# Performance work log

Measured on AMD Instinct MI355X. Metric: run time of the kernel, lower is better.

## Reference

```python
import jax, jax.numpy as jnp
import numpy as np

HIDDEN_DIM = 4096
NUM_SHARDS = 64
TOP_K = 2
B = 16384


def setup_inputs() -> dict:
    key = jax.random.key(0)
    k_h, k_w = jax.random.split(key)
    h = jax.random.normal(k_h, (B, HIDDEN_DIM), dtype=jnp.float32)
    # nn.init.normal_(weight, std=0.02); bias zeros
    weight = jax.random.normal(k_w, (NUM_SHARDS, HIDDEN_DIM), dtype=jnp.float32) * 0.02
    bias = jnp.zeros((NUM_SHARDS,), dtype=jnp.float32)
    return {"h": h, "weight": weight, "bias": bias}


def reference(h, weight, bias):
    # logits: (B, num_shards)
    logits = jnp.einsum("bd,ed->be", h, weight) + bias
    probs = jax.nn.softmax(logits, axis=-1)
    k = min(TOP_K, weight.shape[0])
    topk_vals, topk_idx = jax.lax.top_k(probs, k)
    denom = jnp.maximum(jnp.sum(topk_vals, axis=-1, keepdims=True), 1e-12)
    topk_w = topk_vals / denom
    return topk_w, topk_idx
```

## Files before the change

kernel.cpp:

```cpp
#include <hip/hip_runtime.h>
#include <hip/hip_bf16.h>
#include <math.h>


#define HIDDEN 4096
#define NSHARD 64
#define B_ROWS 16384

typedef short bf16x8 __attribute__((ext_vector_type(8)));
typedef float f32x4  __attribute__((ext_vector_type(4)));

__device__ __forceinline__ unsigned short f32_to_bf16_rn(float f) {
    __hip_bfloat16 h = __float2bfloat16(f);
    return *reinterpret_cast<unsigned short*>(&h);
}
__device__ __forceinline__ float bf16_bits_to_f32(unsigned short u) {
    union { unsigned int i; float f; } v; v.i = ((unsigned int)u) << 16;
    return v.f;
}

__global__ __launch_bounds__(256)
void wsplit_kernel(const float* __restrict__ w,
                   unsigned short* __restrict__ w_hi,
                   unsigned short* __restrict__ w_lo)
{
    const int idx = (blockIdx.x * 256 + threadIdx.x) * 4;
    const float4 v = *(const float4*)(w + idx);
    const float a[4] = {v.x, v.y, v.z, v.w};
    ushort4 hi, lo;
    unsigned short hb;
    hb = f32_to_bf16_rn(a[0]); hi.x = hb; lo.x = f32_to_bf16_rn(a[0] - bf16_bits_to_f32(hb));
    hb = f32_to_bf16_rn(a[1]); hi.y = hb; lo.y = f32_to_bf16_rn(a[1] - bf16_bits_to_f32(hb));
    hb = f32_to_bf16_rn(a[2]); hi.z = hb; lo.z = f32_to_bf16_rn(a[2] - bf16_bits_to_f32(hb));
    hb = f32_to_bf16_rn(a[3]); hi.w = hb; lo.w = f32_to_bf16_rn(a[3] - bf16_bits_to_f32(hb));
    *(ushort4*)(w_hi + idx) = hi;
    *(ushort4*)(w_lo + idx) = lo;
}

__global__ __launch_bounds__(256)
void gate_kernel(const float* __restrict__ h,
                 const unsigned short* __restrict__ w_hi,
                 const unsigned short* __restrict__ w_lo,
                 const float* __restrict__ bias,
                 float* __restrict__ out)
{
    __shared__ float lsum[4][16][68];

    const int tid  = threadIdx.x;
    const int lane = tid & 63;
    const int q    = tid >> 6;
    const int m    = lane & 15;
    const int quad = lane >> 4;
    const int row0 = blockIdx.x * 16;

    const float* __restrict__ aptr =
        h + (size_t)(row0 + m) * HIDDEN + q * 1024 + quad * 8;
    const size_t boff = (size_t)m * HIDDEN + q * 1024 + quad * 8;

    f32x4 acch[4], accx[4];
#pragma unroll
    for (int j = 0; j < 4; ++j) {
        acch[j] = (f32x4)0.0f;
        accx[j] = (f32x4)0.0f;
    }

    for (int step = 0; step < 32; ++step) {
        const float4 a0 = *(const float4*)(aptr + step * 32);
        const float4 a1 = *(const float4*)(aptr + step * 32 + 4);
        const float av[8] = {a0.x, a0.y, a0.z, a0.w, a1.x, a1.y, a1.z, a1.w};
        bf16x8 ahi, alo;
#pragma unroll
        for (int i = 0; i < 8; ++i) {
            const unsigned short hb = f32_to_bf16_rn(av[i]);
            ahi[i] = (short)hb;
            alo[i] = (short)f32_to_bf16_rn(av[i] - bf16_bits_to_f32(hb));
        }
#pragma unroll
        for (int j = 0; j < 4; ++j) {
            const bf16x8 bh = *(const bf16x8*)(w_hi + boff + (size_t)j * 16 * HIDDEN + step * 32);
            const bf16x8 bl = *(const bf16x8*)(w_lo + boff + (size_t)j * 16 * HIDDEN + step * 32);
            acch[j] = __builtin_amdgcn_mfma_f32_16x16x32_bf16(ahi, bh, acch[j], 0, 0, 0);
            accx[j] = __builtin_amdgcn_mfma_f32_16x16x32_bf16(alo, bh, accx[j], 0, 0, 0);
            accx[j] = __builtin_amdgcn_mfma_f32_16x16x32_bf16(ahi, bl, accx[j], 0, 0, 0);
            accx[j] = __builtin_amdgcn_mfma_f32_16x16x32_bf16(alo, bl, accx[j], 0, 0, 0);
        }
    }

#pragma unroll
    for (int j = 0; j < 4; ++j)
#pragma unroll
        for (int p = 0; p < 4; ++p)
            lsum[q][quad * 4 + p][j * 16 + m] = acch[j][p] + accx[j][p];

    __syncthreads();

    const int row = tid >> 4;
    const int s   = tid & 15;
    float4 vs = *(const float4*)&lsum[0][row][s * 4];
    {
        const float4 v1 = *(const float4*)&lsum[1][row][s * 4];
        const float4 v2 = *(const float4*)&lsum[2][row][s * 4];
        const float4 v3 = *(const float4*)&lsum[3][row][s * 4];
        vs.x += v1.x + v2.x + v3.x;
        vs.y += v1.y + v2.y + v3.y;
        vs.z += v1.z + v2.z + v3.z;
        vs.w += v1.w + v2.w + v3.w;
    }
    const float4 bv = *(const float4*)(bias + s * 4);
    const float v0 = vs.x + bv.x, v1 = vs.y + bv.y;
    const float v2 = vs.z + bv.z, v3 = vs.w + bv.w;

    float m1 = v0, m2 = -INFINITY;
    int   i1 = s * 4, i2 = 0;
    if (v1 > m1)      { m2 = m1; i2 = i1; m1 = v1; i1 = s * 4 + 1; }
    else              { m2 = v1; i2 = s * 4 + 1; }
    if (v2 > m1)      { m2 = m1; i2 = i1; m1 = v2; i1 = s * 4 + 2; }
    else if (v2 > m2) { m2 = v2; i2 = s * 4 + 2; }
    if (v3 > m1)      { m2 = m1; i2 = i1; m1 = v3; i1 = s * 4 + 3; }
    else if (v3 > m2) { m2 = v3; i2 = s * 4 + 3; }

#pragma unroll
    for (int msk = 1; msk <= 8; msk <<= 1) {
        const float o1 = __shfl_xor(m1, msk, 64);
        const int   q1 = __shfl_xor(i1, msk, 64);
        const float o2 = __shfl_xor(m2, msk, 64);
        const int   q2 = __shfl_xor(i2, msk, 64);
        const bool take = (o1 > m1) || (o1 == m1 && q1 < i1);
        const float w1 = take ? o1 : m1; const int w1i = take ? q1 : i1;
        const float l1 = take ? m1 : o1; const int l1i = take ? i1 : q1;
        const float s2 = take ? o2 : m2; const int s2i = take ? q2 : i2;
        const bool t2 = (l1 > s2) || (l1 == s2 && l1i < s2i);
        m1 = w1; i1 = w1i;
        m2 = t2 ? l1 : s2; i2 = t2 ? l1i : s2i;
    }

    if (s == 0) {
        const int orow = row0 + row;
        const float ed  = expf(m2 - m1);
        const float inv = 1.0f / (1.0f + ed);
        out[2 * orow + 0] = inv;
        out[2 * orow + 1] = ed * inv;
        float* __restrict__ oidx = out + 2 * B_ROWS;
        oidx[2 * orow + 0] = (float)i1;
        oidx[2 * orow + 1] = (float)i2;
    }
}

extern "C" void kernel_launch(void* const* d_in, const int* in_sizes, int n_in,
                              void* d_out, int out_size, void* d_ws, size_t ws_size,
                              hipStream_t stream)
{
    const float* h    = (const float*)d_in[0];
    const float* wt   = (const float*)d_in[1];
    const float* bias = (const float*)d_in[2];
    float* out = (float*)d_out;

    unsigned short* w_hi = (unsigned short*)d_ws;
    unsigned short* w_lo = w_hi + (size_t)NSHARD * HIDDEN;

    wsplit_kernel<<<dim3(NSHARD * HIDDEN / 1024), dim3(256), 0, stream>>>(wt, w_hi, w_lo);
    gate_kernel<<<dim3(B_ROWS / 16), dim3(256), 0, stream>>>(h, w_hi, w_lo, bias, out);
}
```

Before: 464.9 us.

## Split shard columns across twice the waves and fully unroll K loop

Doubles the block to 512 threads so each wave computes only two of the four 16-column shard tiles, halving the accumulators per wave and raising the number of waves per CU. The K loop is fully unrolled with all B-operand loads hoisted ahead of the split and MFMA work, and the bf16 hi/lo split is done with hand-written integer rounding. The cost is that each A tile is now loaded and split twice, once by each wave in a pair, which adds global traffic and VALU work.

```diff
diff --git a/kernel.cpp b/kernel.cpp
--- a/kernel.cpp
+++ b/kernel.cpp
@@ -19,6 +19,16 @@
     return v.f;
 }
 
+__device__ __forceinline__ void bf16_split(float f, short* hi, short* lo) {
+    const unsigned int u = __float_as_uint(f);
+    const unsigned int r = u + 0x7fffu + ((u >> 16) & 1u);
+    *hi = (short)(r >> 16);
+    union { unsigned int i; float f2; } hv; hv.i = r & 0xffff0000u;
+    const float res = f - hv.f2;
+    const unsigned int u2 = __float_as_uint(res);
+    *lo = (short)((u2 + 0x7fffu + ((u2 >> 16) & 1u)) >> 16);
+}
+
 __global__ __launch_bounds__(256)
 void wsplit_kernel(const float* __restrict__ w,
                    unsigned short* __restrict__ w_hi,
@@ -37,7 +47,7 @@
     *(ushort4*)(w_lo + idx) = lo;
 }
 
-__global__ __launch_bounds__(256)
+__global__ __launch_bounds__(512, 8)
 void gate_kernel(const float* __restrict__ h,
                  const unsigned short* __restrict__ w_hi,
                  const unsigned short* __restrict__ w_lo,
@@ -48,7 +58,9 @@
 
     const int tid  = threadIdx.x;
     const int lane = tid & 63;
-    const int q    = tid >> 6;
+    const int wv   = tid >> 6;
+    const int q    = wv >> 1;
+    const int jh   = wv & 1;
     const int m    = lane & 15;
     const int quad = lane >> 4;
     const int row0 = blockIdx.x * 16;
@@ -56,93 +68,106 @@
     const float* __restrict__ aptr =
         h + (size_t)(row0 + m) * HIDDEN + q * 1024 + quad * 8;
     const size_t boff = (size_t)m * HIDDEN + q * 1024 + quad * 8;
+    const unsigned short* __restrict__ bh0p = w_hi + boff + (size_t)(jh * 2 + 0) * 16 * HIDDEN;
+    const unsigned short* __restrict__ bh1p = w_hi + boff + (size_t)(jh * 2 + 1) * 16 * HIDDEN;
+    const unsigned short* __restrict__ bl0p = w_lo + boff + (size_t)(jh * 2 + 0) * 16 * HIDDEN;
+    const unsigned short* __restrict__ bl1p = w_lo + boff + (size_t)(jh * 2 + 1) * 16 * HIDDEN;
 
-    f32x4 acch[4], accx[4];
+    f32x4 acch[2], accx[2];
 #pragma unroll
-    for (int j = 0; j < 4; ++j) {
+    for (int j = 0; j < 2; ++j) {
         acch[j] = (f32x4)0.0f;
         accx[j] = (f32x4)0.0f;
     }
 
+#pragma unroll
     for (int step = 0; step < 32; ++step) {
         const float4 a0 = *(const float4*)(aptr + step * 32);
         const float4 a1 = *(const float4*)(aptr + step * 32 + 4);
+        const bf16x8 bh0 = *(const bf16x8*)(bh0p + step * 32);
+        const bf16x8 bh1 = *(const bf16x8*)(bh1p + step * 32);
+        const bf16x8 bl0 = *(const bf16x8*)(bl0p + step * 32);
+        const bf16x8 bl1 = *(const bf16x8*)(bl1p + step * 32);
+
         const float av[8] = {a0.x, a0.y, a0.z, a0.w, a1.x, a1.y, a1.z, a1.w};
         bf16x8 ahi, alo;
 #pragma unroll
         for (int i = 0; i < 8; ++i) {
-            const unsigned short hb = f32_to_bf16_rn(av[i]);
-            ahi[i] = (short)hb;
-            alo[i] = (short)f32_to_bf16_rn(av[i] - bf16_bits_to_f32(hb));
+            short hb, lb;
+            bf16_split(av[i], &hb, &lb);
+            ahi[i] = hb;
+            alo[i] = lb;
         }
-#pragma unroll
-        for (int j = 0; j < 4; ++j) {
-            const bf16x8 bh = *(const bf16x8*)(w_hi + boff + (size_t)j * 16 * HIDDEN + step * 32);
-            const bf16x8 bl = *(const bf16x8*)(w_lo + boff + (size_t)j * 16 * HIDDEN + step * 32);
-            acch[j] = __builtin_amdgcn_mfma_f32_16x16x32_bf16(ahi, bh, acch[j], 0, 0, 0);
-            accx[j] = __builtin_amdgcn_mfma_f32_16x16x32_bf16(alo, bh, accx[j], 0, 0, 0);
-            accx[j] = __builtin_amdgcn_mfma_f32_16x16x32_bf16(ahi, bl, accx[j], 0, 0, 0);
-            accx[j] = __builtin_amdgcn_mfma_f32_16x16x32_bf16(alo, bl, accx[j], 0, 0, 0);
-        }
+
+        acch[0] = __builtin_amdgcn_mfma_f32_16x16x32_bf16(ahi, bh0, acch[0], 0, 0, 0);
+        acch[1] = __builtin_amdgcn_mfma_f32_16x16x32_bf16(ahi, bh1, acch[1], 0, 0, 0);
+        accx[0] = __builtin_amdgcn_mfma_f32_16x16x32_bf16(alo, bh0, accx[0], 0, 0, 0);
+        accx[1] = __builtin_amdgcn_mfma_f32_16x16x32_bf16(alo, bh1, accx[1], 0, 0, 0);
+        accx[0] = __builtin_amdgcn_mfma_f32_16x16x32_bf16(ahi, bl0, accx[0], 0, 0, 0);
+        accx[1] = __builtin_amdgcn_mfma_f32_16x16x32_bf16(ahi, bl1, accx[1], 0, 0, 0);
+        accx[0] = __builtin_amdgcn_mfma_f32_16x16x32_bf16(alo, bl0, accx[0], 0, 0, 0);
+        accx[1] = __builtin_amdgcn_mfma_f32_16x16x32_bf16(alo, bl1, accx[1], 0, 0, 0);
     }
 
 #pragma unroll
-    for (int j = 0; j < 4; ++j)
+    for (int j = 0; j < 2; ++j)
 #pragma unroll
         for (int p = 0; p < 4; ++p)
-            lsum[q][quad * 4 + p][j * 16 + m] = acch[j][p] + accx[j][p];
+            lsum[q][quad * 4 + p][(jh * 2 + j) * 16 + m] = acch[j][p] + accx[j][p];
 
     __syncthreads();
 
-    const int row = tid >> 4;
-    const int s   = tid & 15;
-    float4 vs = *(const float4*)&lsum[0][row][s * 4];
-    {
-        const float4 v1 = *(const float4*)&lsum[1][row][s * 4];
-        const float4 v2 = *(const float4*)&lsum[2][row][s * 4];
-        const float4 v3 = *(const float4*)&lsum[3][row][s * 4];
-        vs.x += v1.x + v2.x + v3.x;
-        vs.y += v1.y + v2.y + v3.y;
-        vs.z += v1.z + v2.z + v3.z;
-        vs.w += v1.w + v2.w + v3.w;
-    }
-    const float4 bv = *(const float4*)(bias + s * 4);
-    const float v0 = vs.x + bv.x, v1 = vs.y + bv.y;
-    const float v2 = vs.z + bv.z, v3 = vs.w + bv.w;
+    if (tid < 256) {
+        const int row = tid >> 4;
+        const int s   = tid & 15;
+        float4 vs = *(const float4*)&lsum[0][row][s * 4];
+        {
+            const float4 v1 = *(const float4*)&lsum[1][row][s * 4];
+            const float4 v2 = *(const float4*)&lsum[2][row][s * 4];
+            const float4 v3 = *(const float4*)&lsum[3][row][s * 4];
+            vs.x += v1.x + v2.x + v3.x;
+            vs.y += v1.y + v2.y + v3.y;
+            vs.z += v1.z + v2.z + v3.z;
+            vs.w += v1.w + v2.w + v3.w;
+        }
+        const float4 bv = *(const float4*)(bias + s * 4);
+        const float v0 = vs.x + bv.x, v1 = vs.y + bv.y;
+        const float v2 = vs.z + bv.z, v3 = vs.w + bv.w;
 
-    float m1 = v0, m2 = -INFINITY;
-    int   i1 = s * 4, i2 = 0;
-    if (v1 > m1)      { m2 = m1; i2 = i1; m1 = v1; i1 = s * 4 + 1; }
-    else              { m2 = v1; i2 = s * 4 + 1; }
-    if (v2 > m1)      { m2 = m1; i2 = i1; m1 = v2; i1 = s * 4 + 2; }
-    else if (v2 > m2) { m2 = v2; i2 = s * 4 + 2; }
-    if (v3 > m1)      { m2 = m1; i2 = i1; m1 = v3; i1 = s * 4 + 3; }
-    else if (v3 > m2) { m2 = v3; i2 = s * 4 + 3; }
+        float m1 = v0, m2 = -INFINITY;
+        int   i1 = s * 4, i2 = 0;
+        if (v1 > m1)      { m2 = m1; i2 = i1; m1 = v1; i1 = s * 4 + 1; }
+        else              { m2 = v1; i2 = s * 4 + 1; }
+        if (v2 > m1)      { m2 = m1; i2 = i1; m1 = v2; i1 = s * 4 + 2; }
+        else if (v2 > m2) { m2 = v2; i2 = s * 4 + 2; }
+        if (v3 > m1)      { m2 = m1; i2 = i1; m1 = v3; i1 = s * 4 + 3; }
+        else if (v3 > m2) { m2 = v3; i2 = s * 4 + 3; }
 
 #pragma unroll
-    for (int msk = 1; msk <= 8; msk <<= 1) {
-        const float o1 = __shfl_xor(m1, msk, 64);
-        const int   q1 = __shfl_xor(i1, msk, 64);
-        const float o2 = __shfl_xor(m2, msk, 64);
-        const int   q2 = __shfl_xor(i2, msk, 64);
-        const bool take = (o1 > m1) || (o1 == m1 && q1 < i1);
-        const float w1 = take ? o1 : m1; const int w1i = take ? q1 : i1;
-        const float l1 = take ? m1 : o1; const int l1i = take ? i1 : q1;
-        const float s2 = take ? o2 : m2; const int s2i = take ? q2 : i2;
-        const bool t2 = (l1 > s2) || (l1 == s2 && l1i < s2i);
-        m1 = w1; i1 = w1i;
-        m2 = t2 ? l1 : s2; i2 = t2 ? l1i : s2i;
-    }
+        for (int msk = 1; msk <= 8; msk <<= 1) {
+            const float o1 = __shfl_xor(m1, msk, 64);
+            const int   q1 = __shfl_xor(i1, msk, 64);
+            const float o2 = __shfl_xor(m2, msk, 64);
+            const int   q2 = __shfl_xor(i2, msk, 64);
+            const bool take = (o1 > m1) || (o1 == m1 && q1 < i1);
+            const float w1 = take ? o1 : m1; const int w1i = take ? q1 : i1;
+            const float l1 = take ? m1 : o1; const int l1i = take ? i1 : q1;
+            const float s2 = take ? o2 : m2; const int s2i = take ? q2 : i2;
+            const bool t2 = (l1 > s2) || (l1 == s2 && l1i < s2i);
+            m1 = w1; i1 = w1i;
+            m2 = t2 ? l1 : s2; i2 = t2 ? l1i : s2i;
+        }
 
-    if (s == 0) {
-        const int orow = row0 + row;
-        const float ed  = expf(m2 - m1);
-        const float inv = 1.0f / (1.0f + ed);
-        out[2 * orow + 0] = inv;
-        out[2 * orow + 1] = ed * inv;
-        float* __restrict__ oidx = out + 2 * B_ROWS;
-        oidx[2 * orow + 0] = (float)i1;
-        oidx[2 * orow + 1] = (float)i2;
+        if (s == 0) {
+            const int orow = row0 + row;
+            const float ed  = expf(m2 - m1);
+            const float inv = 1.0f / (1.0f + ed);
+            out[2 * orow + 0] = inv;
+            out[2 * orow + 1] = ed * inv;
+            float* __restrict__ oidx = out + 2 * B_ROWS;
+            oidx[2 * orow + 0] = (float)i1;
+            oidx[2 * orow + 1] = (float)i2;
+        }
     }
 }
 
@@ -159,5 +184,5 @@
     unsigned short* w_lo = w_hi + (size_t)NSHARD * HIDDEN;
 
     wsplit_kernel<<<dim3(NSHARD * HIDDEN / 1024), dim3(256), 0, stream>>>(wt, w_hi, w_lo);
-    gate_kernel<<<dim3(B_ROWS / 16), dim3(256), 0, stream>>>(h, w_hi, w_lo, bias, out);
+    gate_kernel<<<dim3(B_ROWS / 16), dim3(512), 0, stream>>>(h, w_hi, w_lo, bias, out);
 }
```

After: 485.5 us. +4.4%, slower.
